# Performance work log

Measured on AMD Instinct MI355X. Metric: run time of the kernel, lower is better.

Reference implementation:

```python
import jax, jax.numpy as jnp
import numpy as np

N, E, HID, H_SA, H_MHA, L = 20000, 320000, 128, 4, 4, 32
MLP_HID = 4 * HID
EPS = 1e-6


def _ln(x, eps=EPS):
    mu = jnp.mean(x, axis=-1, keepdims=True)
    var = jnp.var(x, axis=-1, keepdims=True)
    return (x - mu) * jax.lax.rsqrt(var + eps)


def _modulate(x, shift, scale):
    return x * (1.0 + scale) + shift


def setup_inputs() -> dict:
    key = jax.random.key(0)
    ks = jax.random.split(key, 32)
    s = 0.02
    inp = {
        'x': jax.random.normal(ks[0], (N, HID), jnp.float32),
        'edge_index': jax.random.randint(ks[1], (2, E), 0, N, jnp.int64),
        't': jax.random.normal(ks[2], (N, HID), jnp.float32),
        'text_emb': jax.random.normal(ks[3], (N, L, HID), jnp.float32),
        # TransformerConv (per-head out_channels = HID, concat=False)
        'sa_q_w': jax.random.normal(ks[4], (HID, H_SA * HID), jnp.float32) * s,
        'sa_q_b': jnp.zeros((H_SA * HID,), jnp.float32),
        'sa_k_w': jax.random.normal(ks[5], (HID, H_SA * HID), jnp.float32) * s,
        'sa_k_b': jnp.zeros((H_SA * HID,), jnp.float32),
        'sa_v_w': jax.random.normal(ks[6], (HID, H_SA * HID), jnp.float32) * s,
        'sa_v_b': jnp.zeros((H_SA * HID,), jnp.float32),
        'sa_skip_w': jax.random.normal(ks[7], (HID, HID), jnp.float32) * s,
        'sa_skip_b': jnp.zeros((HID,), jnp.float32),
        # norm3 affine
        'n3_g': jnp.ones((HID,), jnp.float32),
        'n3_b': jnp.zeros((HID,), jnp.float32),
        # MultiheadAttention
        'mha_q_w': jax.random.normal(ks[8], (HID, HID), jnp.float32) * s,
        'mha_q_b': jnp.zeros((HID,), jnp.float32),
        'mha_k_w': jax.random.normal(ks[9], (HID, HID), jnp.float32) * s,
        'mha_k_b': jnp.zeros((HID,), jnp.float32),
        'mha_v_w': jax.random.normal(ks[10], (HID, HID), jnp.float32) * s,
        'mha_v_b': jnp.zeros((HID,), jnp.float32),
        'mha_o_w': jax.random.normal(ks[11], (HID, HID), jnp.float32) * s,
        'mha_o_b': jnp.zeros((HID,), jnp.float32),
        # MLP
        'fc1_w': jax.random.normal(ks[12], (HID, MLP_HID), jnp.float32) * s,
        'fc1_b': jnp.zeros((MLP_HID,), jnp.float32),
        'fc2_w': jax.random.normal(ks[13], (MLP_HID, HID), jnp.float32) * s,
        'fc2_b': jnp.zeros((HID,), jnp.float32),
        # adaLN modulation
        'ada_w': jax.random.normal(ks[14], (HID, 6 * HID), jnp.float32) * s,
        'ada_b': jnp.zeros((6 * HID,), jnp.float32),
    }
    return inp


def reference(x, edge_index, t, text_emb,
              sa_q_w, sa_q_b, sa_k_w, sa_k_b, sa_v_w, sa_v_b, sa_skip_w, sa_skip_b,
              n3_g, n3_b,
              mha_q_w, mha_q_b, mha_k_w, mha_k_b, mha_v_w, mha_v_b, mha_o_w, mha_o_b,
              fc1_w, fc1_b, fc2_w, fc2_b, ada_w, ada_b):
    n = x.shape[0]
    # adaLN: SiLU -> Linear -> chunk(6)
    mod = jax.nn.silu(t) @ ada_w + ada_b  # [N, 6*HID]
    shift_msa, scale_msa, gate_msa, shift_mlp, scale_mlp, gate_mlp = jnp.split(mod, 6, axis=1)

    # ---- graph self-attention (PyG TransformerConv, concat=False) ----
    xm = _modulate(_ln(x), shift_msa, scale_msa)  # [N, HID]
    q = (xm @ sa_q_w + sa_q_b).reshape(n, H_SA, HID)
    k = (xm @ sa_k_w + sa_k_b).reshape(n, H_SA, HID)
    v = (xm @ sa_v_w + sa_v_b).reshape(n, H_SA, HID)
    src, dst = edge_index[0], edge_index[1]  # messages flow src -> dst
    # per-edge attention logits [E, H]
    logits = jnp.einsum('ehd,ehd->eh', q[dst], k[src]) / jnp.sqrt(jnp.float32(HID))
    m = jax.ops.segment_max(logits, dst, num_segments=n)          # [N, H]
    ex = jnp.exp(logits - m[dst])                                  # [E, H]
    den = jax.ops.segment_sum(ex, dst, num_segments=n)            # [N, H]
    alpha = ex / den[dst]                                          # [E, H]
    agg = jax.ops.segment_sum(alpha[:, :, None] * v[src], dst, num_segments=n)  # [N, H, HID]
    sa_out = agg.mean(axis=1) + (xm @ sa_skip_w + sa_skip_b)       # concat=False -> head mean, + root skip
    x = x + gate_msa * sa_out

    # ---- cross attention: each node attends over its text memory ----
    qn = _ln(x) * n3_g + n3_b                                      # norm3 (affine)
    dh = HID // H_MHA
    qh = (qn @ mha_q_w + mha_q_b).reshape(n, H_MHA, dh)
    kh = (text_emb @ mha_k_w + mha_k_b).reshape(n, L, H_MHA, dh)
    vh = (text_emb @ mha_v_w + mha_v_b).reshape(n, L, H_MHA, dh)
    scores = jnp.einsum('nhd,nlhd->nhl', qh, kh) / jnp.sqrt(jnp.float32(dh))
    attn = jax.nn.softmax(scores, axis=-1)
    ctx = jnp.einsum('nhl,nlhd->nhd', attn, vh).reshape(n, HID)
    x = x + (ctx @ mha_o_w + mha_o_b)

    # ---- gated MLP ----
    xm2 = _modulate(_ln(x), shift_mlp, scale_mlp)
    h = jax.nn.gelu(xm2 @ fc1_w + fc1_b, approximate=True)
    x = x + gate_mlp * (h @ fc2_w + fc2_b)
    return x
```

## Files before the change

kernel.cpp:

```cpp
#include <hip/hip_runtime.h>
#include <hip/hip_bf16.h>
#include <math.h>

using ushort8 = __attribute__((ext_vector_type(8))) unsigned short;
using short8  = __attribute__((ext_vector_type(8))) short;
using f32x4   = __attribute__((ext_vector_type(4))) float;
using f32x2   = __attribute__((ext_vector_type(2))) float;

__device__ __forceinline__ float bf2f(unsigned short u) {
    union { unsigned int i; float f; } c; c.i = ((unsigned int)u) << 16; return c.f;
}
__device__ __forceinline__ unsigned short f2bf(float f) {
    __hip_bfloat16 h = __float2bfloat16(f);
    return *reinterpret_cast<unsigned short*>(&h);
}
__device__ __forceinline__ float silu_f(float x) { return x / (1.f + __expf(-x)); }
__device__ __forceinline__ float gelu_f(float x) {
    float x3 = x * x * x;
    return 0.5f * x * (1.f + tanhf(0.7978845608028654f * (x + 0.044715f * x3)));
}

constexpr int QKV_STRIDE_B = 2304;

__device__ __forceinline__ void stage_tile_async(
    const unsigned short* __restrict__ gbase,
    int K, unsigned short (*lds)[64], int nrows, int wid, int lane)
{
    int nch = nrows >> 3;
#pragma unroll
    for (int c = wid; c < nch; c += 4) {
        int n0 = c * 8;
        int n = n0 + (lane >> 3);
        int b = (lane & 7) ^ (n & 7);
        const unsigned short* src = gbase + (size_t)n * K + b * 8;
        __builtin_amdgcn_global_load_lds(
            (const __attribute__((address_space(1))) unsigned int*)src,
            (__attribute__((address_space(3))) unsigned int*)&lds[n0][0],
            16, 0, 0);
    }
}

template<int WM, int EPI, int OUTBF>
__global__ __launch_bounds__(256) void gemm_mfma(
    const void* __restrict__ Ain, const unsigned short* __restrict__ Wt,
    const float* __restrict__ bias, void* __restrict__ Cout,
    const float* __restrict__ res, const void* __restrict__ gatep,
    void* __restrict__ out2, int Nrows, int K, int M)
{
    constexpr int BM = 32 * WM;
    __shared__ unsigned short As[BM][64];
    __shared__ unsigned short Bs[128][64];
    const int tid = threadIdx.x;
    const int gx = gridDim.x;
    const int T = gx * gridDim.y;
    const int hw = blockIdx.y * gx + blockIdx.x;
    const int q = T >> 3, r = T & 7, xc = hw & 7, j = hw >> 3;
    const int work = (xc < r ? xc * (q + 1) : r * (q + 1) + (xc - r) * q) + j;
    const int row0 = (work / gx) * BM;
    const int col0 = (work % gx) * 128;
    const int lane = tid & 63;
    const int wid  = tid >> 6;
    const int wr = (wid >> 1) * 16 * WM;
    const int wc = (wid & 1) * 64;
    const int lr = lane & 15;
    const int lk = lane >> 4;

    f32x4 acc[WM][4];
#pragma unroll
    for (int i = 0; i < WM; i++)
#pragma unroll
        for (int jj = 0; jj < 4; jj++) acc[i][jj] = (f32x4)0.f;

    for (int k0 = 0; k0 < K; k0 += 64) {
        stage_tile_async((const unsigned short*)Ain + (size_t)row0 * K + k0,
                         K, As, BM, wid, lane);
        stage_tile_async(Wt + (size_t)col0 * K + k0, K, Bs, 128, wid, lane);
        __syncthreads();

        short8 afr[WM][2], bfr[4][2];
#pragma unroll
        for (int fr = 0; fr < WM; fr++)
#pragma unroll
            for (int s = 0; s < 2; s++) {
                int m = wr + fr * 16 + lr;
                int blk = (s * 4 + lk) ^ (m & 7);
                afr[fr][s] = *(const short8*)&As[m][blk * 8];
            }
#pragma unroll
        for (int fc = 0; fc < 4; fc++)
#pragma unroll
            for (int s = 0; s < 2; s++) {
                int n = wc + fc * 16 + lr;
                int blk = (s * 4 + lk) ^ (n & 7);
                bfr[fc][s] = *(const short8*)&Bs[n][blk * 8];
            }
#pragma unroll
        for (int fr = 0; fr < WM; fr++)
#pragma unroll
            for (int fc = 0; fc < 4; fc++)
#pragma unroll
                for (int s = 0; s < 2; s++)
                    acc[fr][fc] = __builtin_amdgcn_mfma_f32_16x16x32_bf16(
                        afr[fr][s], bfr[fc][s], acc[fr][fc], 0, 0, 0);
        __syncthreads();
    }

#pragma unroll
    for (int fr = 0; fr < WM; fr++) {
#pragma unroll
        for (int fc = 0; fc < 4; fc++) {
#pragma unroll
            for (int rr = 0; rr < 4; rr++) {
                int lrow = wr + fr * 16 + (lane >> 4) * 4 + rr;
                int row = row0 + lrow;
                if (row >= Nrows) continue;
                int col = col0 + wc + fc * 16 + (lane & 15);
                float val = acc[fr][fc][rr] + bias[col];
                if (EPI == 4) {
                    unsigned char* rowp = (unsigned char*)Cout + (size_t)row * QKV_STRIDE_B;
                    if (col < 512) {
                        *(unsigned short*)(rowp + 2 * col) = f2bf(val);
                    } else if (col < 1536) {
                        int p = __builtin_amdgcn_cvt_pk_fp8_f32(val, 0.f, 0, false);
                        rowp[1024 + (col - 512)] = (unsigned char)(p & 0xff);
                    } else {
                        *(unsigned short*)(rowp + 2048 + 2 * (col - 1536)) = f2bf(val);
                    }
                } else if (EPI == 5) {
                    size_t idx = (size_t)row * M + col;
                    float x2 = res[idx] + val;
                    ((float*)Cout)[idx] = x2;
                    (&Bs[0][0])[lrow * 128 + col - col0] = f2bf(x2);
                } else {
                    size_t idx = (size_t)row * M + col;
                    if (EPI == 1) val = gelu_f(val);
                    else if (EPI == 2) val = res[idx] + val;
                    else if (EPI == 3) val = res[idx] +
                        bf2f(((const unsigned short*)gatep)[(size_t)row * 768 + col]) * val;
                    if (OUTBF) ((unsigned short*)Cout)[idx] = f2bf(val);
                    else       ((float*)Cout)[idx] = val;
                }
            }
        }
    }

    if constexpr (EPI == 5) {
        __syncthreads();
        const unsigned short* x2b = &Bs[0][0];
        const unsigned short* mod = (const unsigned short*)gatep;
        for (int rr = wid; rr < BM; rr += 4) {
            int row = row0 + rr;
            if (row >= Nrows) continue;
            ushort2 xv = *(const ushort2*)&x2b[rr * 128 + lane * 2];
            float v0 = bf2f(xv.x), v1 = bf2f(xv.y);
            float s = v0 + v1, ss = v0 * v0 + v1 * v1;
#pragma unroll
            for (int mm = 1; mm < 64; mm <<= 1) {
                s += __shfl_xor(s, mm); ss += __shfl_xor(ss, mm);
            }
            float mu = s * (1.f / 128.f);
            float rs = rsqrtf(ss * (1.f / 128.f) - mu * mu + 1e-6f);
            const unsigned short* mp = mod + (size_t)row * 768;
            ushort2 sh = *(const ushort2*)(mp + 384 + lane * 2);
            ushort2 sc = *(const ushort2*)(mp + 512 + lane * 2);
            ushort2 o;
            o.x = f2bf((v0 - mu) * rs * (1.f + bf2f(sc.x)) + bf2f(sh.x));
            o.y = f2bf((v1 - mu) * rs * (1.f + bf2f(sc.y)) + bf2f(sh.y));
            *(ushort2*)((unsigned short*)out2 + (size_t)row * 128 + lane * 2) = o;
        }
    }
}

__global__ __launch_bounds__(256) void silu_bf16_kernel(
    const float* __restrict__ t, unsigned short* __restrict__ o, int n8)
{
    int i = blockIdx.x * 256 + threadIdx.x;
    if (i >= n8) return;
    const float* p = t + (size_t)i * 8;
    float4 a = *(const float4*)p, b = *(const float4*)(p + 4);
    float v[8] = {a.x, a.y, a.z, a.w, b.x, b.y, b.z, b.w};
    ushort8 h;
#pragma unroll
    for (int jj = 0; jj < 8; jj++) h[jj] = f2bf(silu_f(v[jj]));
    *(ushort8*)(o + (size_t)i * 8) = h;
}

__global__ __launch_bounds__(256) void prep_all(
    const float* __restrict__ qW, const float* __restrict__ qB,
    const float* __restrict__ kW, const float* __restrict__ kB,
    const float* __restrict__ vW, const float* __restrict__ vB,
    const float* __restrict__ sW, const float* __restrict__ sB,
    const float* __restrict__ f1W, const float* __restrict__ f2W,
    const float* __restrict__ adW,
    unsigned short* __restrict__ Wsa_t, float* __restrict__ bsa,
    unsigned short* __restrict__ fc1_t, unsigned short* __restrict__ fc2_t,
    unsigned short* __restrict__ ada_t,
    const float* __restrict__ Wq, const float* __restrict__ bq,
    const float* __restrict__ Wk, const float* __restrict__ Wv,
    const float* __restrict__ bv, const float* __restrict__ Wo,
    const float* __restrict__ bo,
    unsigned short* __restrict__ Mcat_t, float* __restrict__ biasM,
    unsigned short* __restrict__ Pcat_t, float* __restrict__ co)
{
    int g = blockIdx.x * 256 + threadIdx.x;
    if (g < 65536) {
        int m = g >> 7, kk = g & 127;
        Wsa_t[m * 128 + kk] = f2bf(qW[(size_t)kk * 512 + m]);
        if (kk == 0) bsa[m] = qB[m];
    } else if (g < 131072) {
        int l = g - 65536; int m = l >> 7, kk = l & 127;
        int h = m >> 7, dl = m & 127;
        int p = 512 + h * 256 + ((dl >> 3) << 4) + (dl & 7);
        Wsa_t[p * 128 + kk] = f2bf(kW[(size_t)kk * 512 + m]);
        if (kk == 0) bsa[p] = kB[m];
    } else if (g < 196608) {
        int l = g - 131072; int m = l >> 7, kk = l & 127;
        int h = m >> 7, dl = m & 127;
        int p = 512 + h * 256 + ((dl >> 3) << 4) + 8 + (dl & 7);
        Wsa_t[p * 128 + kk] = f2bf(vW[(size_t)kk * 512 + m]);
        if (kk == 0) bsa[p] = vB[m];
    } else if (g < 212992) {
        int l = g - 196608; int m = l >> 7, kk = l & 127;
        Wsa_t[(1536 + m) * 128 + kk] = f2bf(sW[(size_t)kk * 128 + m]);
        if (kk == 0) bsa[1536 + m] = sB[m];
    } else if (g < 278528) {
        int l = g - 212992; int m = l >> 7, kk = l & 127;
        fc1_t[m * 128 + kk] = f2bf(f1W[(size_t)kk * 512 + m]);
    } else if (g < 344064) {
        int l = g - 278528; int m = l >> 9, kk = l & 511;
        fc2_t[m * 512 + kk] = f2bf(f2W[(size_t)kk * 128 + m]);
    } else if (g < 442368) {
        int l = g - 344064; int m = l >> 7, kk = l & 127;
        ada_t[m * 128 + kk] = f2bf(adW[(size_t)kk * 768 + m]);
    } else {
        int g2 = g - 442368;
        {
            int i0 = g2 >> 9, col = g2 & 511, h = col >> 7, i = col & 127;
            float s = 0.f;
#pragma unroll 8
            for (int jj = 0; jj < 32; jj++)
                s += Wq[i0 * 128 + h * 32 + jj] * Wk[i * 128 + h * 32 + jj];
            Mcat_t[col * 128 + i0] = f2bf(s);
        }
        {
            int rowp = g2 >> 7, jc = g2 & 127, h = rowp >> 7, i = rowp & 127;
            float s = 0.f;
#pragma unroll 8
            for (int d = 0; d < 32; d++)
                s += Wv[i * 128 + h * 32 + d] * Wo[(h * 32 + d) * 128 + jc];
            Pcat_t[jc * 512 + rowp] = f2bf(s);
        }
        if (g2 < 512) {
            int h = g2 >> 7, i = g2 & 127;
            float s = 0.f;
            for (int jj = 0; jj < 32; jj++)
                s += bq[h * 32 + jj] * Wk[i * 128 + h * 32 + jj];
            biasM[g2] = s;
        }
        if (g2 < 128) {
            float s = bo[g2];
            for (int m = 0; m < 128; m++) s += bv[m] * Wo[m * 128 + g2];
            co[g2] = s;
        }
    }
}

__global__ __launch_bounds__(256) void ln_mod_kernel(
    const float* __restrict__ x, const unsigned short* __restrict__ mod,
    int shift_off, int scale_off, unsigned short* __restrict__ outb, int N)
{
    int node = blockIdx.x * 4 + (threadIdx.x >> 6);
    if (node >= N) return;
    int lane = threadIdx.x & 63;
    f32x2 v = *(const f32x2*)(x + (size_t)node * 128 + lane * 2);
    float s = v[0] + v[1], ss = v[0] * v[0] + v[1] * v[1];
#pragma unroll
    for (int m = 1; m < 64; m <<= 1) { s += __shfl_xor(s, m); ss += __shfl_xor(ss, m); }
    float mu = s * (1.f / 128.f);
    float rs = rsqrtf(ss * (1.f / 128.f) - mu * mu + 1e-6f);
    const unsigned short* mp = mod + (size_t)node * 768;
    ushort2 sh = *(const ushort2*)(mp + shift_off + lane * 2);
    ushort2 sc = *(const ushort2*)(mp + scale_off + lane * 2);
    ushort2 o;
    o.x = f2bf((v[0] - mu) * rs * (1.f + bf2f(sc.x)) + bf2f(sh.x));
    o.y = f2bf((v[1] - mu) * rs * (1.f + bf2f(sc.y)) + bf2f(sh.y));
    *(ushort2*)(outb + (size_t)node * 128 + lane * 2) = o;
}

__global__ void count_edges(const int* __restrict__ dst, int* __restrict__ count, int E) {
    int e = blockIdx.x * blockDim.x + threadIdx.x;
    if (e < E) atomicAdd(&count[dst[e]], 1);
}

__global__ __launch_bounds__(1024) void scan_block(const int* __restrict__ cnt,
                                                   int* __restrict__ pre,
                                                   int* __restrict__ bsum, int n)
{
    __shared__ int tmp[1024];
    int gid = blockIdx.x * 1024 + threadIdx.x;
    int v = (gid < n) ? cnt[gid] : 0;
    tmp[threadIdx.x] = v;
    __syncthreads();
    for (int off = 1; off < 1024; off <<= 1) {
        int add = (threadIdx.x >= off) ? tmp[threadIdx.x - off] : 0;
        __syncthreads();
        tmp[threadIdx.x] += add;
        __syncthreads();
    }
    if (gid < n) pre[gid] = tmp[threadIdx.x];
    if (threadIdx.x == 1023) bsum[blockIdx.x] = tmp[1023];
}

__global__ void scan_fix(const int* __restrict__ pre, const int* __restrict__ bsum,
                         const int* __restrict__ cnt,
                         int* __restrict__ base, int* __restrict__ cursor,
                         int n, int nb)
{
    __shared__ int boff[32];
    if (threadIdx.x == 0) {
        int c = 0;
        for (int i = 0; i < nb; i++) { boff[i] = c; c += bsum[i]; }
    }
    __syncthreads();
    int gid = blockIdx.x * 256 + threadIdx.x;
    if (gid < n) {
        int inc = pre[gid] + boff[gid >> 10];
        base[gid + 1] = inc;
        cursor[gid] = inc - cnt[gid];
    }
    if (gid == 0) base[0] = 0;
}

__global__ void scatter_edges(const int* __restrict__ src, const int* __restrict__ dst,
                              int* __restrict__ cursor, int* __restrict__ csr_src, int E) {
    int e = blockIdx.x * blockDim.x + threadIdx.x;
    if (e < E) {
        int pos = atomicAdd(&cursor[dst[e]], 1);
        csr_src[pos] = src[e];
    }
}

__global__ __launch_bounds__(64) void sa_node_kernel(
    const unsigned char* __restrict__ qkv,
    const int* __restrict__ base, const int* __restrict__ csr_src,
    const float* __restrict__ x, const unsigned short* __restrict__ mod,
    const float* __restrict__ n3g, const float* __restrict__ n3b,
    float* __restrict__ x1, unsigned short* __restrict__ qn)
{
    int node = blockIdx.x, l = threadIdx.x;
    const unsigned char* nrow = qkv + (size_t)node * QKV_STRIDE_B;
    ushort8 qu = *(const ushort8*)(nrow + l * 16);
    const float scl = 0.08838834764831845f;
    float q[8];
#pragma unroll
    for (int jj = 0; jj < 8; jj++) q[jj] = bf2f(qu[jj]) * scl;
    int beg = base[node], end = base[node + 1];
    float den = 0.f;
    float a[8];
#pragma unroll
    for (int jj = 0; jj < 8; jj++) a[jj] = 0.f;
    uint4 c0 = make_uint4(0, 0, 0, 0), c1 = c0;
    if (beg < end)
        c0 = *(const uint4*)(qkv + (size_t)csr_src[beg] * QKV_STRIDE_B + 1024 + l * 16);
    if (beg + 1 < end)
        c1 = *(const uint4*)(qkv + (size_t)csr_src[beg + 1] * QKV_STRIDE_B + 1024 + l * 16);
    for (int e = beg; e < end; e += 2) {
        uint4 m0 = c0, m1 = c1;
        if (e + 2 < end)
            c0 = *(const uint4*)(qkv + (size_t)csr_src[e + 2] * QKV_STRIDE_B + 1024 + l * 16);
        if (e + 3 < end)
            c1 = *(const uint4*)(qkv + (size_t)csr_src[e + 3] * QKV_STRIDE_B + 1024 + l * 16);
        f32x2 kA, kB, kC, kD;
        kA = __builtin_amdgcn_cvt_pk_f32_fp8(m0.x, false);
        kB = __builtin_amdgcn_cvt_pk_f32_fp8(m0.x, true);
        kC = __builtin_amdgcn_cvt_pk_f32_fp8(m0.y, false);
        kD = __builtin_amdgcn_cvt_pk_f32_fp8(m0.y, true);
        float p0 = q[0]*kA[0] + q[1]*kA[1] + q[2]*kB[0] + q[3]*kB[1]
                 + q[4]*kC[0] + q[5]*kC[1] + q[6]*kD[0] + q[7]*kD[1];
        kA = __builtin_amdgcn_cvt_pk_f32_fp8(m1.x, false);
        kB = __builtin_amdgcn_cvt_pk_f32_fp8(m1.x, true);
        kC = __builtin_amdgcn_cvt_pk_f32_fp8(m1.y, false);
        kD = __builtin_amdgcn_cvt_pk_f32_fp8(m1.y, true);
        float p1 = q[0]*kA[0] + q[1]*kA[1] + q[2]*kB[0] + q[3]*kB[1]
                 + q[4]*kC[0] + q[5]*kC[1] + q[6]*kD[0] + q[7]*kD[1];
#pragma unroll
        for (int mm = 1; mm < 16; mm <<= 1) {
            p0 += __shfl_xor(p0, mm);
            p1 += __shfl_xor(p1, mm);
        }
        float pe0 = __expf(fminf(p0, 80.f));
        float pe1 = (e + 1 < end) ? __expf(fminf(p1, 80.f)) : 0.f;
        den += pe0 + pe1;
        f32x2 vA, vB, vC, vD, wA, wB, wC, wD;
        vA = __builtin_amdgcn_cvt_pk_f32_fp8(m0.z, false);
        vB = __builtin_amdgcn_cvt_pk_f32_fp8(m0.z, true);
        vC = __builtin_amdgcn_cvt_pk_f32_fp8(m0.w, false);
        vD = __builtin_amdgcn_cvt_pk_f32_fp8(m0.w, true);
        wA = __builtin_amdgcn_cvt_pk_f32_fp8(m1.z, false);
        wB = __builtin_amdgcn_cvt_pk_f32_fp8(m1.z, true);
        wC = __builtin_amdgcn_cvt_pk_f32_fp8(m1.w, false);
        wD = __builtin_amdgcn_cvt_pk_f32_fp8(m1.w, true);
        a[0] += pe0 * vA[0] + pe1 * wA[0];
        a[1] += pe0 * vA[1] + pe1 * wA[1];
        a[2] += pe0 * vB[0] + pe1 * wB[0];
        a[3] += pe0 * vB[1] + pe1 * wB[1];
        a[4] += pe0 * vC[0] + pe1 * wC[0];
        a[5] += pe0 * vC[1] + pe1 * wC[1];
        a[6] += pe0 * vD[0] + pe1 * wD[0];
        a[7] += pe0 * vD[1] + pe1 * wD[1];
    }
    float inv = (den > 0.f) ? 0.25f / den : 0.f;
    __shared__ float sa_sh[128];
#pragma unroll
    for (int jj = 0; jj < 8; jj++) {
        float s = a[jj] * inv;
        s += __shfl_xor(s, 16);
        s += __shfl_xor(s, 32);
        a[jj] = s;
    }
    if (l < 16) {
#pragma unroll
        for (int jj = 0; jj < 8; jj++) sa_sh[l * 8 + jj] = a[jj];
    }
    __syncthreads();
    f32x2 sa2 = *(const f32x2*)&sa_sh[l * 2];
    ushort2 sk = *(const ushort2*)(nrow + 2048 + l * 4);
    ushort2 gt = *(const ushort2*)(mod + (size_t)node * 768 + 256 + l * 2);
    f32x2 xv2 = *(const f32x2*)(x + (size_t)node * 128 + l * 2);
    float xv0 = xv2[0] + bf2f(gt.x) * (sa2[0] + bf2f(sk.x));
    float xv1 = xv2[1] + bf2f(gt.y) * (sa2[1] + bf2f(sk.y));
    f32x2 xo; xo[0] = xv0; xo[1] = xv1;
    *(f32x2*)(x1 + (size_t)node * 128 + l * 2) = xo;
    float s = xv0 + xv1, ssq = xv0 * xv0 + xv1 * xv1;
#pragma unroll
    for (int m = 1; m < 64; m <<= 1) { s += __shfl_xor(s, m); ssq += __shfl_xor(ssq, m); }
    float mu = s * (1.f / 128.f);
    float rs = rsqrtf(ssq * (1.f / 128.f) - mu * mu + 1e-6f);
    ushort2 qo;
    qo.x = f2bf((xv0 - mu) * rs * n3g[l * 2] + n3b[l * 2]);
    qo.y = f2bf((xv1 - mu) * rs * n3g[l * 2 + 1] + n3b[l * 2 + 1]);
    *(ushort2*)(qn + (size_t)node * 128 + l * 2) = qo;
}

__global__ __launch_bounds__(128) void cross_mid_kernel(
    const float* __restrict__ te, const unsigned short* __restrict__ qw,
    unsigned short* __restrict__ u)
{
    int node = blockIdx.x, t = threadIdx.x;
    __shared__ float tes[32 * 132];
    __shared__ float qws[512];
    __shared__ float attnL[128];
#pragma unroll
    for (int i = 0; i < 8; i++) {
        int f = t + i * 128;
        int l = f >> 5, ii = (f & 31) * 4;
        float4 val = *(const float4*)(te + (size_t)node * 4096 + l * 128 + ii);
        *(float4*)&tes[l * 132 + ii] = val;
    }
    {
        ushort4 qv = *(const ushort4*)(qw + (size_t)node * 512 + t * 4);
        qws[t * 4 + 0] = bf2f(qv.x);
        qws[t * 4 + 1] = bf2f(qv.y);
        qws[t * 4 + 2] = bf2f(qv.z);
        qws[t * 4 + 3] = bf2f(qv.w);
    }
    __syncthreads();

    int h = t >> 5, l = t & 31;
    float sc = 0.f;
#pragma unroll
    for (int i = 0; i < 32; i++) {
        float4 tv = *(const float4*)&tes[l * 132 + i * 4];
        float4 qv4 = *(const float4*)&qws[h * 128 + i * 4];
        sc += tv.x * qv4.x + tv.y * qv4.y + tv.z * qv4.z + tv.w * qv4.w;
    }
    sc *= 0.17677669529663687f;
    float mx = sc;
#pragma unroll
    for (int mm = 1; mm < 32; mm <<= 1) mx = fmaxf(mx, __shfl_xor(mx, mm));
    float e = __expf(sc - mx);
    float ssum = e;
#pragma unroll
    for (int mm = 1; mm < 32; mm <<= 1) ssum += __shfl_xor(ssum, mm);
    attnL[t] = e / ssum;
    __syncthreads();

    int i0 = t & 31;
    float u0 = 0, u1 = 0, u2 = 0, u3 = 0;
#pragma unroll 4
    for (int ll = 0; ll < 32; ll++) {
        float a = attnL[h * 32 + ll];
        u0 += a * tes[ll * 132 + i0];
        u1 += a * tes[ll * 132 + i0 + 32];
        u2 += a * tes[ll * 132 + i0 + 64];
        u3 += a * tes[ll * 132 + i0 + 96];
    }
    size_t ub = (size_t)node * 512 + h * 128;
    u[ub + i0] = f2bf(u0);
    u[ub + i0 + 32] = f2bf(u1);
    u[ub + i0 + 64] = f2bf(u2);
    u[ub + i0 + 96] = f2bf(u3);
}

extern "C" void kernel_launch(void* const* d_in, const int* in_sizes, int n_in,
                              void* d_out, int out_size, void* d_ws, size_t ws_size,
                              hipStream_t stream)
{
    const int N = in_sizes[0] / 128;
    const int E = in_sizes[1] / 2;

    const float* x      = (const float*)d_in[0];
    const int*   ei     = (const int*)d_in[1];
    const float* t_in   = (const float*)d_in[2];
    const float* te     = (const float*)d_in[3];
    const float* sa_q_w = (const float*)d_in[4];
    const float* sa_q_b = (const float*)d_in[5];
    const float* sa_k_w = (const float*)d_in[6];
    const float* sa_k_b = (const float*)d_in[7];
    const float* sa_v_w = (const float*)d_in[8];
    const float* sa_v_b = (const float*)d_in[9];
    const float* sa_skip_w = (const float*)d_in[10];
    const float* sa_skip_b = (const float*)d_in[11];
    const float* n3_g   = (const float*)d_in[12];
    const float* n3_b   = (const float*)d_in[13];
    const float* mha_q_w = (const float*)d_in[14];
    const float* mha_q_b = (const float*)d_in[15];
    const float* mha_k_w = (const float*)d_in[16];
    const float* mha_v_w = (const float*)d_in[18];
    const float* mha_v_b = (const float*)d_in[19];
    const float* mha_o_w = (const float*)d_in[20];
    const float* mha_o_b = (const float*)d_in[21];
    const float* fc1_w  = (const float*)d_in[22];
    const float* fc1_b  = (const float*)d_in[23];
    const float* fc2_w  = (const float*)d_in[24];
    const float* fc2_b  = (const float*)d_in[25];
    const float* ada_w  = (const float*)d_in[26];
    const float* ada_b  = (const float*)d_in[27];
    float* out = (float*)d_out;

    float* ws = (float*)d_ws;
    size_t o = 0;
    unsigned short* modb = (unsigned short*)(ws + o); o += (size_t)N * 384;
    unsigned short* Bbuf = (unsigned short*)(ws + o); o += (size_t)N * 64;
    unsigned short* Qn   = (unsigned short*)(ws + o); o += (size_t)N * 64;
    unsigned short* Cbuf = (unsigned short*)(ws + o); o += (size_t)N * 256;
    unsigned short* Dbuf = (unsigned short*)(ws + o); o += (size_t)N * 256;
    unsigned short* Ebuf = (unsigned short*)(ws + o); o += (size_t)N * 256;
    float* Gbuf = ws + o; o += (size_t)N * 128;
    unsigned char* QKV = (unsigned char*)(ws + o); o += (size_t)N * (QKV_STRIDE_B / 4);
    unsigned short* Wsa_t  = (unsigned short*)(ws + o); o += 1664 * 128 / 2;
    unsigned short* Mcat_t = (unsigned short*)(ws + o); o += 512 * 128 / 2;
    unsigned short* Pcat_t = (unsigned short*)(ws + o); o += 128 * 512 / 2;
    unsigned short* fc1_t  = (unsigned short*)(ws + o); o += 512 * 128 / 2;
    unsigned short* fc2_t  = (unsigned short*)(ws + o); o += 128 * 512 / 2;
    unsigned short* ada_t  = (unsigned short*)(ws + o); o += 768 * 128 / 2;
    float* bsa   = ws + o; o += 1664;
    float* biasM = ws + o; o += 512;
    float* co    = ws + o; o += 128;
    int* count   = (int*)(ws + o); o += N;
    int* base    = (int*)(ws + o); o += N + 4;
    int* cursor  = (int*)(ws + o); o += N;
    int* pre     = (int*)(ws + o); o += N;
    int* bsum    = (int*)(ws + o); o += 32;
    int* csr_src = (int*)(ws + o); o += E;

    unsigned short* Tbuf = Ebuf;

    const int* src = ei;
    const int* dst = ei + E;
    const int rb128 = (N + 127) / 128;
    const int rb64  = (N + 63) / 64;
    const int nScan = (N + 1023) / 1024;

    prep_all<<<1984, 256, 0, stream>>>(sa_q_w, sa_q_b, sa_k_w, sa_k_b,
                                       sa_v_w, sa_v_b, sa_skip_w, sa_skip_b,
                                       fc1_w, fc2_w, ada_w,
                                       Wsa_t, bsa, fc1_t, fc2_t, ada_t,
                                       mha_q_w, mha_q_b, mha_k_w, mha_v_w,
                                       mha_v_b, mha_o_w, mha_o_b,
                                       Mcat_t, biasM, Pcat_t, co);

    hipMemsetAsync(count, 0, (size_t)N * sizeof(int), stream);
    count_edges<<<(E + 255) / 256, 256, 0, stream>>>(dst, count, E);
    scan_block<<<nScan, 1024, 0, stream>>>(count, pre, bsum, N);
    scan_fix<<<(N + 255) / 256, 256, 0, stream>>>(pre, bsum, count, base, cursor, N, nScan);
    scatter_edges<<<(E + 255) / 256, 256, 0, stream>>>(src, dst, cursor, csr_src, E);

    silu_bf16_kernel<<<(N * 16 + 255) / 256, 256, 0, stream>>>(t_in, Tbuf, N * 16);

    gemm_mfma<4, 0, 1><<<dim3(6, rb128), 256, 0, stream>>>(
        Tbuf, ada_t, ada_b, modb, nullptr, nullptr, nullptr, N, 128, 768);

    ln_mod_kernel<<<(N + 3) / 4, 256, 0, stream>>>(x, modb, 0, 128, Bbuf, N);

    gemm_mfma<4, 4, 1><<<dim3(13, rb128), 256, 0, stream>>>(
        Bbuf, Wsa_t, bsa, QKV, nullptr, nullptr, nullptr, N, 128, 1664);

    sa_node_kernel<<<N, 64, 0, stream>>>(QKV, base, csr_src, x, modb,
                                         n3_g, n3_b, Gbuf, Qn);

    gemm_mfma<4, 0, 1><<<dim3(4, rb128), 256, 0, stream>>>(
        Qn, Mcat_t, biasM, Cbuf, nullptr, nullptr, nullptr, N, 128, 512);
    cross_mid_kernel<<<N, 128, 0, stream>>>(te, Cbuf, Dbuf);
    gemm_mfma<2, 5, 0><<<dim3(1, rb64), 256, 0, stream>>>(
        Dbuf, Pcat_t, co, Gbuf, Gbuf, modb, Bbuf, N, 512, 128);

    gemm_mfma<4, 1, 1><<<dim3(4, rb128), 256, 0, stream>>>(
        Bbuf, fc1_t, fc1_b, Ebuf, nullptr, nullptr, nullptr, N, 128, 512);
    gemm_mfma<2, 3, 0><<<dim3(1, rb64), 256, 0, stream>>>(
        Ebuf, fc2_t, fc2_b, out, Gbuf, modb + 640, nullptr, N, 512, 128);
}
```

Baseline: 365.2 us.

## Store SA queries and cross-attn projections in fp8, fuse SiLU into prep, warp-shuffle scan

```diff
diff --git a/kernel.cpp b/kernel.cpp
--- a/kernel.cpp
+++ b/kernel.cpp
@@ -14,13 +14,17 @@
     __hip_bfloat16 h = __float2bfloat16(f);
     return *reinterpret_cast<unsigned short*>(&h);
 }
+__device__ __forceinline__ unsigned char f2fp8(float f) {
+    int p = __builtin_amdgcn_cvt_pk_fp8_f32(f, 0.f, 0, false);
+    return (unsigned char)(p & 0xff);
+}
 __device__ __forceinline__ float silu_f(float x) { return x / (1.f + __expf(-x)); }
 __device__ __forceinline__ float gelu_f(float x) {
     float x3 = x * x * x;
     return 0.5f * x * (1.f + tanhf(0.7978845608028654f * (x + 0.044715f * x3)));
 }
 
-constexpr int QKV_STRIDE_B = 2304;
+constexpr int QKV_STRIDE_B = 1792;
 
 __device__ __forceinline__ void stage_tile_async(
     const unsigned short* __restrict__ gbase,
@@ -118,19 +122,18 @@
                 float val = acc[fr][fc][rr] + bias[col];
                 if (EPI == 4) {
                     unsigned char* rowp = (unsigned char*)Cout + (size_t)row * QKV_STRIDE_B;
-                    if (col < 512) {
-                        *(unsigned short*)(rowp + 2 * col) = f2bf(val);
-                    } else if (col < 1536) {
-                        int p = __builtin_amdgcn_cvt_pk_fp8_f32(val, 0.f, 0, false);
-                        rowp[1024 + (col - 512)] = (unsigned char)(p & 0xff);
+                    if (col < 1536) {
+                        rowp[col] = f2fp8(val);
                     } else {
-                        *(unsigned short*)(rowp + 2048 + 2 * (col - 1536)) = f2bf(val);
+                        *(unsigned short*)(rowp + 1536 + 2 * (col - 1536)) = f2bf(val);
                     }
                 } else if (EPI == 5) {
                     size_t idx = (size_t)row * M + col;
                     float x2 = res[idx] + val;
                     ((float*)Cout)[idx] = x2;
                     (&Bs[0][0])[lrow * 128 + col - col0] = f2bf(x2);
+                } else if (EPI == 6) {
+                    ((unsigned char*)Cout)[(size_t)row * M + col] = f2fp8(val);
                 } else {
                     size_t idx = (size_t)row * M + col;
                     if (EPI == 1) val = gelu_f(val);
@@ -169,20 +172,6 @@
             *(ushort2*)((unsigned short*)out2 + (size_t)row * 128 + lane * 2) = o;
         }
     }
-}
-
-__global__ __launch_bounds__(256) void silu_bf16_kernel(
-    const float* __restrict__ t, unsigned short* __restrict__ o, int n8)
-{
-    int i = blockIdx.x * 256 + threadIdx.x;
-    if (i >= n8) return;
-    const float* p = t + (size_t)i * 8;
-    float4 a = *(const float4*)p, b = *(const float4*)(p + 4);
-    float v[8] = {a.x, a.y, a.z, a.w, b.x, b.y, b.z, b.w};
-    ushort8 h;
-#pragma unroll
-    for (int jj = 0; jj < 8; jj++) h[jj] = f2bf(silu_f(v[jj]));
-    *(ushort8*)(o + (size_t)i * 8) = h;
 }
 
 __global__ __launch_bounds__(256) void prep_all(
@@ -200,7 +189,8 @@
     const float* __restrict__ bv, const float* __restrict__ Wo,
     const float* __restrict__ bo,
     unsigned short* __restrict__ Mcat_t, float* __restrict__ biasM,
-    unsigned short* __restrict__ Pcat_t, float* __restrict__ co)
+    unsigned short* __restrict__ Pcat_t, float* __restrict__ co,
+    const float* __restrict__ t_in, unsigned short* __restrict__ Tbuf, int n8)
 {
     int g = blockIdx.x * 256 + threadIdx.x;
     if (g < 65536) {
@@ -232,7 +222,7 @@
     } else if (g < 442368) {
         int l = g - 344064; int m = l >> 7, kk = l & 127;
         ada_t[m * 128 + kk] = f2bf(adW[(size_t)kk * 768 + m]);
-    } else {
+    } else if (g < 507904) {
         int g2 = g - 442368;
         {
             int i0 = g2 >> 9, col = g2 & 511, h = col >> 7, i = col & 127;
@@ -261,6 +251,17 @@
             float s = bo[g2];
             for (int m = 0; m < 128; m++) s += bv[m] * Wo[m * 128 + g2];
             co[g2] = s;
+        }
+    } else {
+        int i = g - 507904;
+        if (i < n8) {
+            const float* p = t_in + (size_t)i * 8;
+            float4 a = *(const float4*)p, b = *(const float4*)(p + 4);
+            float v[8] = {a.x, a.y, a.z, a.w, b.x, b.y, b.z, b.w};
+            ushort8 h;
+#pragma unroll
+            for (int jj = 0; jj < 8; jj++) h[jj] = f2bf(silu_f(v[jj]));
+            *(ushort8*)(Tbuf + (size_t)i * 8) = h;
         }
     }
 }
@@ -296,19 +297,30 @@
                                                    int* __restrict__ pre,
                                                    int* __restrict__ bsum, int n)
 {
-    __shared__ int tmp[1024];
     int gid = blockIdx.x * 1024 + threadIdx.x;
-    int v = (gid < n) ? cnt[gid] : 0;
-    tmp[threadIdx.x] = v;
+    int lane = threadIdx.x & 63, w = threadIdx.x >> 6;
+    int s = (gid < n) ? cnt[gid] : 0;
+#pragma unroll
+    for (int off = 1; off < 64; off <<= 1) {
+        int t = __shfl_up(s, off);
+        if (lane >= off) s += t;
+    }
+    __shared__ int wsum[16];
+    if (lane == 63) wsum[w] = s;
     __syncthreads();
-    for (int off = 1; off < 1024; off <<= 1) {
-        int add = (threadIdx.x >= off) ? tmp[threadIdx.x - off] : 0;
-        __syncthreads();
-        tmp[threadIdx.x] += add;
-        __syncthreads();
-    }
-    if (gid < n) pre[gid] = tmp[threadIdx.x];
-    if (threadIdx.x == 1023) bsum[blockIdx.x] = tmp[1023];
+    if (w == 0 && lane < 16) {
+        int wsv = wsum[lane];
+#pragma unroll
+        for (int off = 1; off < 16; off <<= 1) {
+            int t = __shfl_up(wsv, off);
+            if (lane >= off) wsv += t;
+        }
+        wsum[lane] = wsv;
+    }
+    __syncthreads();
+    if (w > 0) s += wsum[w - 1];
+    if (gid < n) pre[gid] = s;
+    if (threadIdx.x == 1023) bsum[blockIdx.x] = s;
 }
 
 __global__ void scan_fix(const int* __restrict__ pre, const int* __restrict__ bsum,
@@ -349,11 +361,19 @@
 {
     int node = blockIdx.x, l = threadIdx.x;
     const unsigned char* nrow = qkv + (size_t)node * QKV_STRIDE_B;
-    ushort8 qu = *(const ushort8*)(nrow + l * 16);
+    uint2 qb = *(const uint2*)(nrow + l * 8);
     const float scl = 0.08838834764831845f;
     float q[8];
-#pragma unroll
-    for (int jj = 0; jj < 8; jj++) q[jj] = bf2f(qu[jj]) * scl;
+    {
+        f32x2 qA = __builtin_amdgcn_cvt_pk_f32_fp8(qb.x, false);
+        f32x2 qB = __builtin_amdgcn_cvt_pk_f32_fp8(qb.x, true);
+        f32x2 qC = __builtin_amdgcn_cvt_pk_f32_fp8(qb.y, false);
+        f32x2 qD = __builtin_amdgcn_cvt_pk_f32_fp8(qb.y, true);
+        q[0] = qA[0] * scl; q[1] = qA[1] * scl;
+        q[2] = qB[0] * scl; q[3] = qB[1] * scl;
+        q[4] = qC[0] * scl; q[5] = qC[1] * scl;
+        q[6] = qD[0] * scl; q[7] = qD[1] * scl;
+    }
     int beg = base[node], end = base[node + 1];
     float den = 0.f;
     float a[8];
@@ -361,15 +381,15 @@
     for (int jj = 0; jj < 8; jj++) a[jj] = 0.f;
     uint4 c0 = make_uint4(0, 0, 0, 0), c1 = c0;
     if (beg < end)
-        c0 = *(const uint4*)(qkv + (size_t)csr_src[beg] * QKV_STRIDE_B + 1024 + l * 16);
+        c0 = *(const uint4*)(qkv + (size_t)csr_src[beg] * QKV_STRIDE_B + 512 + l * 16);
     if (beg + 1 < end)
-        c1 = *(const uint4*)(qkv + (size_t)csr_src[beg + 1] * QKV_STRIDE_B + 1024 + l * 16);
+        c1 = *(const uint4*)(qkv + (size_t)csr_src[beg + 1] * QKV_STRIDE_B + 512 + l * 16);
     for (int e = beg; e < end; e += 2) {
         uint4 m0 = c0, m1 = c1;
         if (e + 2 < end)
-            c0 = *(const uint4*)(qkv + (size_t)csr_src[e + 2] * QKV_STRIDE_B + 1024 + l * 16);
+            c0 = *(const uint4*)(qkv + (size_t)csr_src[e + 2] * QKV_STRIDE_B + 512 + l * 16);
         if (e + 3 < end)
-            c1 = *(const uint4*)(qkv + (size_t)csr_src[e + 3] * QKV_STRIDE_B + 1024 + l * 16);
+            c1 = *(const uint4*)(qkv + (size_t)csr_src[e + 3] * QKV_STRIDE_B + 512 + l * 16);
         f32x2 kA, kB, kC, kD;
         kA = __builtin_amdgcn_cvt_pk_f32_fp8(m0.x, false);
         kB = __builtin_amdgcn_cvt_pk_f32_fp8(m0.x, true);
@@ -424,7 +444,7 @@
     }
     __syncthreads();
     f32x2 sa2 = *(const f32x2*)&sa_sh[l * 2];
-    ushort2 sk = *(const ushort2*)(nrow + 2048 + l * 4);
+    ushort2 sk = *(const ushort2*)(nrow + 1536 + l * 4);
     ushort2 gt = *(const ushort2*)(mod + (size_t)node * 768 + 256 + l * 2);
     f32x2 xv2 = *(const f32x2*)(x + (size_t)node * 128 + l * 2);
     float xv0 = xv2[0] + bf2f(gt.x) * (sa2[0] + bf2f(sk.x));
@@ -443,7 +463,7 @@
 }
 
 __global__ __launch_bounds__(128) void cross_mid_kernel(
-    const float* __restrict__ te, const unsigned short* __restrict__ qw,
+    const float* __restrict__ te, const unsigned char* __restrict__ qw,
     unsigned short* __restrict__ u)
 {
     int node = blockIdx.x, t = threadIdx.x;
@@ -458,11 +478,13 @@
         *(float4*)&tes[l * 132 + ii] = val;
     }
     {
-        ushort4 qv = *(const ushort4*)(qw + (size_t)node * 512 + t * 4);
-        qws[t * 4 + 0] = bf2f(qv.x);
-        qws[t * 4 + 1] = bf2f(qv.y);
-        qws[t * 4 + 2] = bf2f(qv.z);
-        qws[t * 4 + 3] = bf2f(qv.w);
+        unsigned int qv = *(const unsigned int*)(qw + (size_t)node * 512 + t * 4);
+        f32x2 a = __builtin_amdgcn_cvt_pk_f32_fp8(qv, false);
+        f32x2 b = __builtin_amdgcn_cvt_pk_f32_fp8(qv, true);
+        qws[t * 4 + 0] = a[0];
+        qws[t * 4 + 1] = a[1];
+        qws[t * 4 + 2] = b[0];
+        qws[t * 4 + 3] = b[1];
     }
     __syncthreads();
 
@@ -543,7 +565,7 @@
     unsigned short* modb = (unsigned short*)(ws + o); o += (size_t)N * 384;
     unsigned short* Bbuf = (unsigned short*)(ws + o); o += (size_t)N * 64;
     unsigned short* Qn   = (unsigned short*)(ws + o); o += (size_t)N * 64;
-    unsigned short* Cbuf = (unsigned short*)(ws + o); o += (size_t)N * 256;
+    unsigned char*  Cbuf = (unsigned char*)(ws + o); o += (size_t)N * 128;
     unsigned short* Dbuf = (unsigned short*)(ws + o); o += (size_t)N * 256;
     unsigned short* Ebuf = (unsigned short*)(ws + o); o += (size_t)N * 256;
     float* Gbuf = ws + o; o += (size_t)N * 128;
@@ -571,14 +593,17 @@
     const int rb128 = (N + 127) / 128;
     const int rb64  = (N + 63) / 64;
     const int nScan = (N + 1023) / 1024;
-
-    prep_all<<<1984, 256, 0, stream>>>(sa_q_w, sa_q_b, sa_k_w, sa_k_b,
-                                       sa_v_w, sa_v_b, sa_skip_w, sa_skip_b,
-                                       fc1_w, fc2_w, ada_w,
-                                       Wsa_t, bsa, fc1_t, fc2_t, ada_t,
-                                       mha_q_w, mha_q_b, mha_k_w, mha_v_w,
-                                       mha_v_b, mha_o_w, mha_o_b,
-                                       Mcat_t, biasM, Pcat_t, co);
+    const int n8 = N * 16;
+    const int prepBlocks = 1984 + (n8 + 255) / 256;
+
+    prep_all<<<prepBlocks, 256, 0, stream>>>(sa_q_w, sa_q_b, sa_k_w, sa_k_b,
+                                             sa_v_w, sa_v_b, sa_skip_w, sa_skip_b,
+                                             fc1_w, fc2_w, ada_w,
+                                             Wsa_t, bsa, fc1_t, fc2_t, ada_t,
+                                             mha_q_w, mha_q_b, mha_k_w, mha_v_w,
+                                             mha_v_b, mha_o_w, mha_o_b,
+                                             Mcat_t, biasM, Pcat_t, co,
+                                             t_in, Tbuf, n8);
 
     hipMemsetAsync(count, 0, (size_t)N * sizeof(int), stream);
     count_edges<<<(E + 255) / 256, 256, 0, stream>>>(dst, count, E);
@@ -586,8 +611,6 @@
     scan_fix<<<(N + 255) / 256, 256, 0, stream>>>(pre, bsum, count, base, cursor, N, nScan);
     scatter_edges<<<(E + 255) / 256, 256, 0, stream>>>(src, dst, cursor, csr_src, E);
 
-    silu_bf16_kernel<<<(N * 16 + 255) / 256, 256, 0, stream>>>(t_in, Tbuf, N * 16);
-
     gemm_mfma<4, 0, 1><<<dim3(6, rb128), 256, 0, stream>>>(
         Tbuf, ada_t, ada_b, modb, nullptr, nullptr, nullptr, N, 128, 768);
 
@@ -599,7 +622,7 @@
     sa_node_kernel<<<N, 64, 0, stream>>>(QKV, base, csr_src, x, modb,
                                          n3_g, n3_b, Gbuf, Qn);
 
-    gemm_mfma<4, 0, 1><<<dim3(4, rb128), 256, 0, stream>>>(
+    gemm_mfma<4, 6, 0><<<dim3(4, rb128), 256, 0, stream>>>(
         Qn, Mcat_t, biasM, Cbuf, nullptr, nullptr, nullptr, N, 128, 512);
     cross_mid_kernel<<<N, 128, 0, stream>>>(te, Cbuf, Dbuf);
     gemm_mfma<2, 5, 0><<<dim3(1, rb64), 256, 0, stream>>>(
```

Measured after the change: 354.9 us, median of 2. -2.8%, faster.
